# Optimization experiments

Measured on AMD Instinct MI355X. Metric: run time of the kernel, lower is better.

Reference implementation:

```python
import jax, jax.numpy as jnp
import numpy as np

B, C, H, W_ = 4, 3, 224, 224
K = 196          # max_segments
E = 768          # embed_dim


def setup_inputs() -> dict:
    key = jax.random.key(0)
    k1, k2, k3 = jax.random.split(key, 3)
    img = jax.random.normal(k1, (B, C, H, W_), dtype=jnp.float32)
    segments = jax.random.randint(k2, (B, H, W_), 0, K, dtype=jnp.int32)
    W = jax.random.normal(k3, (C, E), dtype=jnp.float32) * 0.02
    b = jnp.zeros((E,), dtype=jnp.float32)
    return {"img": img, "segments": segments, "W": W, "b": b}


def reference(img, segments, W, b):
    # Per-segment one-hot masked bucketing (the torch loop, vectorized):
    # segment_features[b,k,c,h,w] = img[b,c,h,w] * (segments[b,h,w] == k)
    onehot = jax.nn.one_hot(segments, K, dtype=img.dtype)           # (B,H,W,K)
    seg_feat = jnp.einsum('bhwk,bchw->bkchw', onehot, img)          # (B,K,C,H,W)
    # Feature extractor stand-in: spatial mean pool + linear C->E
    pooled = seg_feat.mean(axis=(3, 4))                              # (B,K,C)
    out = jnp.einsum('bkc,ce->bke', pooled, W) + b                   # (B,K,E)
    return out
```

## Files before the change

kernel.cpp:

```cpp
#include <hip/hip_runtime.h>

#define Bn  4
#define Cn  3
#define Hn  224
#define Wn  224
#define Kn  196
#define En  768
#define HW  (Hn * Wn)
#define BPB 49
#define NPOOL (Bn * BPB)
#define KC  (Kn * Cn)

__global__ __launch_bounds__(256) void seg_pool_partial(
    const float* __restrict__ img,
    const int*   __restrict__ seg,
    float*       __restrict__ partialsT)
{
    __shared__ float acc[2][KC];
    const int tid = threadIdx.x;
    for (int i = tid; i < 2 * KC; i += 256) ((float*)acc)[i] = 0.0f;
    __syncthreads();

    const int batch = blockIdx.x / BPB;
    const int blk   = blockIdx.x % BPB;
    const int p4    = blk * 256 + tid;
    const int h     = tid >> 7;

    const int4*   seg4 = (const int4*)(seg + (size_t)batch * HW);
    const float4* im   = (const float4*)(img + (size_t)batch * Cn * HW);

    const int4   s  = seg4[p4];
    const float4 v0 = im[p4];
    const float4 v1 = im[HW / 4 + p4];
    const float4 v2 = im[2 * (HW / 4) + p4];

    float* a = acc[h];
    atomicAdd(&a[s.x * 3 + 0], v0.x);
    atomicAdd(&a[s.x * 3 + 1], v1.x);
    atomicAdd(&a[s.x * 3 + 2], v2.x);
    atomicAdd(&a[s.y * 3 + 0], v0.y);
    atomicAdd(&a[s.y * 3 + 1], v1.y);
    atomicAdd(&a[s.y * 3 + 2], v2.y);
    atomicAdd(&a[s.z * 3 + 0], v0.z);
    atomicAdd(&a[s.z * 3 + 1], v1.z);
    atomicAdd(&a[s.z * 3 + 2], v2.z);
    atomicAdd(&a[s.w * 3 + 0], v0.w);
    atomicAdd(&a[s.w * 3 + 1], v1.w);
    atomicAdd(&a[s.w * 3 + 2], v2.w);
    __syncthreads();

    float* dst = partialsT + (size_t)batch * KC * BPB + blk;
    for (int sidx = tid; sidx < KC; sidx += 256)
        dst[(size_t)sidx * BPB] = acc[0][sidx] + acc[1][sidx];
}

__global__ __launch_bounds__(256) void embed_kernel(
    const float* __restrict__ partialsT,
    const float* __restrict__ Wm,
    const float* __restrict__ bias,
    float*       __restrict__ out)
{
    const int tid  = threadIdx.x;
    const int lane = tid & 63;
    const int wv   = tid >> 6;
    const int b    = blockIdx.x / BPB;
    const int k    = (blockIdx.x % BPB) * 4 + wv;

    const float* row = partialsT + ((size_t)b * KC + k * 3) * BPB;
    float a0 = (lane < BPB) ? row[lane]           : 0.0f;
    float a1 = (lane < BPB) ? row[BPB + lane]     : 0.0f;
    float a2 = (lane < BPB) ? row[2 * BPB + lane] : 0.0f;

    #pragma unroll
    for (int off = 32; off > 0; off >>= 1) {
        a0 += __shfl_xor(a0, off, 64);
        a1 += __shfl_xor(a1, off, 64);
        a2 += __shfl_xor(a2, off, 64);
    }
    const float p0 = a0 * (1.0f / (float)HW);
    const float p1 = a1 * (1.0f / (float)HW);
    const float p2 = a2 * (1.0f / (float)HW);

    const float4* W4 = (const float4*)Wm;
    const float4* B4 = (const float4*)bias;
    float4* O4 = (float4*)out + ((size_t)b * Kn + k) * (En / 4);

    #pragma unroll
    for (int part = 0; part < 3; ++part) {
        const int idx = part * 64 + lane;
        const float4 w0 = W4[idx];
        const float4 w1 = W4[192 + idx];
        const float4 w2 = W4[384 + idx];
        const float4 bb = B4[idx];
        float4 r;
        r.x = p0 * w0.x + p1 * w1.x + p2 * w2.x + bb.x;
        r.y = p0 * w0.y + p1 * w1.y + p2 * w2.y + bb.y;
        r.z = p0 * w0.z + p1 * w1.z + p2 * w2.z + bb.z;
        r.w = p0 * w0.w + p1 * w1.w + p2 * w2.w + bb.w;
        O4[idx] = r;
    }
}

extern "C" void kernel_launch(void* const* d_in, const int* in_sizes, int n_in,
                              void* d_out, int out_size, void* d_ws, size_t ws_size,
                              hipStream_t stream) {
    const float* img  = (const float*)d_in[0];
    const int*   seg  = (const int*)  d_in[1];
    const float* Wm   = (const float*)d_in[2];
    const float* bias = (const float*)d_in[3];
    float* out       = (float*)d_out;
    float* partialsT = (float*)d_ws;

    seg_pool_partial<<<NPOOL, 256, 0, stream>>>(img, seg, partialsT);
    embed_kernel<<<NPOOL, 256, 0, stream>>>(partialsT, Wm, bias, out);
}
```

Measured before the change: 67.00 us.

## Fuse pooling and embedding kernels with per-batch global counter barrier

Merges the segment pooling and embedding kernels into one launch. Blocks of the same batch synchronize through a global atomic counter spin-barrier before reading the partial sums. This removes one kernel launch and the gap between launches. In exchange it relies on all 196 blocks being co-resident, and adds spin-wait and fence overhead.

```diff
diff --git a/kernel.cpp b/kernel.cpp
--- a/kernel.cpp
+++ b/kernel.cpp
@@ -11,93 +11,107 @@
 #define NPOOL (Bn * BPB)
 #define KC  (Kn * Cn)
 
-__global__ __launch_bounds__(256) void seg_pool_partial(
+__device__ unsigned int g_cnt[Bn];
+
+__global__ __launch_bounds__(256) void fused_seg_embed(
     const float* __restrict__ img,
     const int*   __restrict__ seg,
+    const float* __restrict__ Wm,
+    const float* __restrict__ bias,
+    float*       __restrict__ out,
     float*       __restrict__ partialsT)
 {
     __shared__ float acc[2][KC];
-    const int tid = threadIdx.x;
+    const int tid  = threadIdx.x;
+    const int lane = tid & 63;
+    const int wv   = tid >> 6;
+
     for (int i = tid; i < 2 * KC; i += 256) ((float*)acc)[i] = 0.0f;
     __syncthreads();
 
     const int batch = blockIdx.x / BPB;
     const int blk   = blockIdx.x % BPB;
-    const int p4    = blk * 256 + tid;
-    const int h     = tid >> 7;
 
-    const int4*   seg4 = (const int4*)(seg + (size_t)batch * HW);
-    const float4* im   = (const float4*)(img + (size_t)batch * Cn * HW);
+    {
+        const int p4 = blk * 256 + tid;
+        const int h  = tid >> 7;
 
-    const int4   s  = seg4[p4];
-    const float4 v0 = im[p4];
-    const float4 v1 = im[HW / 4 + p4];
-    const float4 v2 = im[2 * (HW / 4) + p4];
+        const int4*   seg4 = (const int4*)(seg + (size_t)batch * HW);
+        const float4* im   = (const float4*)(img + (size_t)batch * Cn * HW);
 
-    float* a = acc[h];
-    atomicAdd(&a[s.x * 3 + 0], v0.x);
-    atomicAdd(&a[s.x * 3 + 1], v1.x);
-    atomicAdd(&a[s.x * 3 + 2], v2.x);
-    atomicAdd(&a[s.y * 3 + 0], v0.y);
-    atomicAdd(&a[s.y * 3 + 1], v1.y);
-    atomicAdd(&a[s.y * 3 + 2], v2.y);
-    atomicAdd(&a[s.z * 3 + 0], v0.z);
-    atomicAdd(&a[s.z * 3 + 1], v1.z);
-    atomicAdd(&a[s.z * 3 + 2], v2.z);
-    atomicAdd(&a[s.w * 3 + 0], v0.w);
-    atomicAdd(&a[s.w * 3 + 1], v1.w);
-    atomicAdd(&a[s.w * 3 + 2], v2.w);
+        const int4   s  = seg4[p4];
+        const float4 v0 = im[p4];
+        const float4 v1 = im[HW / 4 + p4];
+        const float4 v2 = im[2 * (HW / 4) + p4];
+
+        float* a = acc[h];
+        atomicAdd(&a[s.x * 3 + 0], v0.x);
+        atomicAdd(&a[s.x * 3 + 1], v1.x);
+        atomicAdd(&a[s.x * 3 + 2], v2.x);
+        atomicAdd(&a[s.y * 3 + 0], v0.y);
+        atomicAdd(&a[s.y * 3 + 1], v1.y);
+        atomicAdd(&a[s.y * 3 + 2], v2.y);
+        atomicAdd(&a[s.z * 3 + 0], v0.z);
+        atomicAdd(&a[s.z * 3 + 1], v1.z);
+        atomicAdd(&a[s.z * 3 + 2], v2.z);
+        atomicAdd(&a[s.w * 3 + 0], v0.w);
+        atomicAdd(&a[s.w * 3 + 1], v1.w);
+        atomicAdd(&a[s.w * 3 + 2], v2.w);
+        __syncthreads();
+
+        float* dst = partialsT + (size_t)batch * KC * BPB + blk;
+        for (int sidx = tid; sidx < KC; sidx += 256)
+            dst[(size_t)sidx * BPB] = acc[0][sidx] + acc[1][sidx];
+    }
+
+    __syncthreads();
+    if (tid == 0) {
+        __threadfence();
+        unsigned old    = atomicAdd(&g_cnt[batch], 1u);
+        unsigned target = old - (old % BPB) + BPB;
+        while (__hip_atomic_load(&g_cnt[batch], __ATOMIC_RELAXED,
+                                 __HIP_MEMORY_SCOPE_AGENT) < target)
+            __builtin_amdgcn_s_sleep(2);
+        __threadfence();
+    }
     __syncthreads();
 
-    float* dst = partialsT + (size_t)batch * KC * BPB + blk;
-    for (int sidx = tid; sidx < KC; sidx += 256)
-        dst[(size_t)sidx * BPB] = acc[0][sidx] + acc[1][sidx];
-}
+    {
+        const int k = blk * 4 + wv;
 
-__global__ __launch_bounds__(256) void embed_kernel(
-    const float* __restrict__ partialsT,
-    const float* __restrict__ Wm,
-    const float* __restrict__ bias,
-    float*       __restrict__ out)
-{
-    const int tid  = threadIdx.x;
-    const int lane = tid & 63;
-    const int wv   = tid >> 6;
-    const int b    = blockIdx.x / BPB;
-    const int k    = (blockIdx.x % BPB) * 4 + wv;
+        const float* row = partialsT + ((size_t)batch * KC + k * 3) * BPB;
+        float a0 = (lane < BPB) ? row[lane]           : 0.0f;
+        float a1 = (lane < BPB) ? row[BPB + lane]     : 0.0f;
+        float a2 = (lane < BPB) ? row[2 * BPB + lane] : 0.0f;
 
-    const float* row = partialsT + ((size_t)b * KC + k * 3) * BPB;
-    float a0 = (lane < BPB) ? row[lane]           : 0.0f;
-    float a1 = (lane < BPB) ? row[BPB + lane]     : 0.0f;
-    float a2 = (lane < BPB) ? row[2 * BPB + lane] : 0.0f;
+        #pragma unroll
+        for (int off = 32; off > 0; off >>= 1) {
+            a0 += __shfl_xor(a0, off, 64);
+            a1 += __shfl_xor(a1, off, 64);
+            a2 += __shfl_xor(a2, off, 64);
+        }
+        const float p0 = a0 * (1.0f / (float)HW);
+        const float p1 = a1 * (1.0f / (float)HW);
+        const float p2 = a2 * (1.0f / (float)HW);
 
-    #pragma unroll
-    for (int off = 32; off > 0; off >>= 1) {
-        a0 += __shfl_xor(a0, off, 64);
-        a1 += __shfl_xor(a1, off, 64);
-        a2 += __shfl_xor(a2, off, 64);
-    }
-    const float p0 = a0 * (1.0f / (float)HW);
-    const float p1 = a1 * (1.0f / (float)HW);
-    const float p2 = a2 * (1.0f / (float)HW);
+        const float4* W4 = (const float4*)Wm;
+        const float4* B4 = (const float4*)bias;
+        float4* O4 = (float4*)out + ((size_t)batch * Kn + k) * (En / 4);
 
-    const float4* W4 = (const float4*)Wm;
-    const float4* B4 = (const float4*)bias;
-    float4* O4 = (float4*)out + ((size_t)b * Kn + k) * (En / 4);
-
-    #pragma unroll
-    for (int part = 0; part < 3; ++part) {
-        const int idx = part * 64 + lane;
-        const float4 w0 = W4[idx];
-        const float4 w1 = W4[192 + idx];
-        const float4 w2 = W4[384 + idx];
-        const float4 bb = B4[idx];
-        float4 r;
-        r.x = p0 * w0.x + p1 * w1.x + p2 * w2.x + bb.x;
-        r.y = p0 * w0.y + p1 * w1.y + p2 * w2.y + bb.y;
-        r.z = p0 * w0.z + p1 * w1.z + p2 * w2.z + bb.z;
-        r.w = p0 * w0.w + p1 * w1.w + p2 * w2.w + bb.w;
-        O4[idx] = r;
+        #pragma unroll
+        for (int part = 0; part < 3; ++part) {
+            const int idx = part * 64 + lane;
+            const float4 w0 = W4[idx];
+            const float4 w1 = W4[192 + idx];
+            const float4 w2 = W4[384 + idx];
+            const float4 bb = B4[idx];
+            float4 r;
+            r.x = p0 * w0.x + p1 * w1.x + p2 * w2.x + bb.x;
+            r.y = p0 * w0.y + p1 * w1.y + p2 * w2.y + bb.y;
+            r.z = p0 * w0.z + p1 * w1.z + p2 * w2.z + bb.z;
+            r.w = p0 * w0.w + p1 * w1.w + p2 * w2.w + bb.w;
+            O4[idx] = r;
+        }
     }
 }
 
@@ -111,6 +125,5 @@
     float* out       = (float*)d_out;
     float* partialsT = (float*)d_ws;
 
-    seg_pool_partial<<<NPOOL, 256, 0, stream>>>(img, seg, partialsT);
-    embed_kernel<<<NPOOL, 256, 0, stream>>>(partialsT, Wm, bias, out);
+    fused_seg_embed<<<NPOOL, 256, 0, stream>>>(img, seg, Wm, bias, out, partialsT);
 }
```

Measured after the change: 84.17 us. +25.6%, slower.
